# Optimization experiments

Hardware: AMD Instinct MI355X
Metric: run time of the kernel (lower is better)

## Reference

```python
import jax, jax.numpy as jnp
import numpy as np

DIMS = [1024, 2048, 2048, 51]
B, P = 16, 1024


def setup_inputs() -> dict:
    key = jax.random.key(0)
    ks = jax.random.split(key, 1 + 2 * (len(DIMS) - 1))
    inp = {
        "num_pairs": P,
        "classifier_input": jax.random.normal(ks[0], (B, P, DIMS[0]), dtype=jnp.float32),
        "num_batches": B,
    }
    # Linear params, PyTorch-style: W[out, in], b[out]
    for li in range(len(DIMS) - 1):
        fan_in = DIMS[li]
        bound = 1.0 / np.sqrt(fan_in)
        inp[f"W{li}"] = jax.random.uniform(ks[1 + 2 * li], (DIMS[li + 1], fan_in), minval=-bound, maxval=bound, dtype=jnp.float32)
        inp[f"b{li}"] = jax.random.uniform(ks[2 + 2 * li], (DIMS[li + 1],), minval=-bound, maxval=bound, dtype=jnp.float32)
    return inp


def reference(num_pairs, classifier_input, num_batches, W0, b0, W1, b1, W2, b2):
    # Batched MLP over all (num_batches * num_pairs) vectors at once.
    # Original loops per (b, i); math is identical. dropout p=0.0 -> identity.
    x = classifier_input  # [B, P, d_in]
    x = jax.nn.relu(jnp.einsum("bpd,hd->bph", x, W0) + b0)
    x = jax.nn.relu(jnp.einsum("bpd,hd->bph", x, W1) + b1)
    out = jnp.einsum("bpd,od->bpo", x, W2) + b2  # [B, P, n_classes]
    return out
```

## Files before the change

### kernel.cpp

```cpp
#include <hip/hip_runtime.h>
#include <hip/hip_bf16.h>
#include <stdint.h>

typedef __attribute__((ext_vector_type(8))) short short8;
typedef __attribute__((ext_vector_type(8))) uint16_t ushort8;
typedef __attribute__((ext_vector_type(4))) float floatx4;

#define TK 32


__device__ __forceinline__ uint16_t f2bf_bits(float f) {
    uint32_t u = __builtin_bit_cast(uint32_t, f);
    u += 0x7FFFu + ((u >> 16) & 1u);
    return (uint16_t)(u >> 16);
}

__device__ __forceinline__ void async_copy16(const void* g, void* l) {
    auto gp = (const __attribute__((address_space(1))) uint32_t*)(uintptr_t)g;
    auto lp = (__attribute__((address_space(3))) uint32_t*)(uint32_t)(uintptr_t)l;
    __builtin_amdgcn_global_load_lds(gp, lp, 16, 0, 0);
}

__device__ __forceinline__ void cvt8_one(const float* __restrict__ s, uint16_t* __restrict__ d) {
    floatx4 a = *(const floatx4*)(s);
    floatx4 b = *(const floatx4*)(s + 4);
    ushort8 o;
#pragma unroll
    for (int k = 0; k < 4; k++) { o[k] = f2bf_bits(a[k]); o[k + 4] = f2bf_bits(b[k]); }
    *(ushort8*)(d) = o;
}


__global__ void cvt8(const float* __restrict__ src, uint16_t* __restrict__ dst, int n) {
    int i = (blockIdx.x * 256 + threadIdx.x) * 8;
    if (i < n) cvt8_one(src + i, dst + i);
}

__global__ void cvt_weights(const float* __restrict__ W0, const float* __restrict__ W1,
                            const float* __restrict__ W2,
                            uint16_t* __restrict__ o0, uint16_t* __restrict__ o1,
                            uint16_t* __restrict__ o2) {
    int i = (blockIdx.x * 256 + threadIdx.x) * 8;
    if (i < 2097152) {
        cvt8_one(W0 + i, o0 + i);
    } else if (i < 2097152 + 4194304) {
        int j = i - 2097152;
        cvt8_one(W1 + j, o1 + j);
    } else {
        int j = i - 6291456;
        if (j < 131072) {
            int row = j >> 11;
            if (row < 51) cvt8_one(W2 + j, o2 + j);
            else { ushort8 z = {0,0,0,0,0,0,0,0}; *(ushort8*)(o2 + j) = z; }
        }
    }
}

__global__ void init_bias(const float* __restrict__ b2, float* __restrict__ out, int n) {
    int i = blockIdx.x * 256 + threadIdx.x;
    if (i < n) out[i] = b2[i % 51];
}


template <int MI, int NJ, int SPLITK, bool RELU, bool OUTF32, bool ATOMIC>
__global__ __launch_bounds__(256, 2)
void gemm_bt(const uint16_t* __restrict__ A,
             const uint16_t* __restrict__ W,
             const float* __restrict__ bias,
             void* __restrict__ out,
             int M, int N, int lda, int kspan, int ldc, int nstore)
{
    constexpr int TMv = MI * 32;
    constexpr int TNv = NJ * 32;
    constexpr int ACH = TMv / 64;
    constexpr int BCH = TNv / 64;

    __shared__ alignas(16) uint16_t sA[2][TMv * TK];
    __shared__ alignas(16) uint16_t sB[2][TNv * TK];

    const int tid  = threadIdx.x;
    const int wave = tid >> 6;
    const int lane = tid & 63;

    const int f = blockIdx.x;
    int m0, n0, kbeg;
    if constexpr (SPLITK > 1) {
        kbeg = (f % SPLITK) * kspan;
        m0   = (f / SPLITK) * TMv;
        n0   = 0;
    } else {
        kbeg = 0;
        const int xcd = f & 7;
        const int loc = f >> 3;
        const int per = (int)gridDim.x >> 3;
        const int nt  = N / TNv;
        n0 = (loc % nt) * TNv;
        m0 = (xcd * (per / nt) + loc / nt) * TMv;
    }

    floatx4 acc[MI][NJ];
    const floatx4 zero = {0.f, 0.f, 0.f, 0.f};
#pragma unroll
    for (int i = 0; i < MI; i++)
#pragma unroll
        for (int j = 0; j < NJ; j++) acc[i][j] = zero;

    const int wr = (wave >> 1) * MI * 16;
    const int wc = (wave & 1) * NJ * 16;

    const int sr   = lane >> 2;
    const int scol = ((lane & 3) ^ ((lane >> 3) & 3)) * 8;

    const uint16_t* ap[ACH];
    const uint16_t* bp[BCH];
#pragma unroll
    for (int t = 0; t < ACH; t++)
        ap[t] = A + (size_t)(m0 + (wave + 4 * t) * 16 + sr) * lda + kbeg + scol;
#pragma unroll
    for (int t = 0; t < BCH; t++)
        bp[t] = W + (size_t)(n0 + (wave + 4 * t) * 16 + sr) * lda + kbeg + scol;

    auto prefetch = [&](int buf) {
#pragma unroll
        for (int t = 0; t < ACH; t++) {
            async_copy16(ap[t], &sA[buf][(wave + 4 * t) * 512]);
            ap[t] += TK;
        }
#pragma unroll
        for (int t = 0; t < BCH; t++) {
            async_copy16(bp[t], &sB[buf][(wave + 4 * t) * 512]);
            bp[t] += TK;
        }
    };

    const int fm = lane & 15;
    const int slot = ((lane >> 4) ^ ((fm >> 1) & 3)) * 8;

    auto compute = [&](int buf) {
        short8 af[MI], bfr[NJ];
#pragma unroll
        for (int i = 0; i < MI; i++)
            af[i] = *(const short8*)(&sA[buf][(wr + i * 16 + fm) * TK + slot]);
#pragma unroll
        for (int j = 0; j < NJ; j++)
            bfr[j] = *(const short8*)(&sB[buf][(wc + j * 16 + fm) * TK + slot]);
#pragma unroll
        for (int i = 0; i < MI; i++)
#pragma unroll
            for (int j = 0; j < NJ; j++)
                acc[i][j] = __builtin_amdgcn_mfma_f32_16x16x32_bf16(af[i], bfr[j], acc[i][j], 0, 0, 0);
    };

    const int niter = kspan / TK;
    prefetch(0);
    for (int it = 0; it < niter; it += 2) {
        __syncthreads();
        if (it + 1 < niter) prefetch(1);
        compute(0);
        __syncthreads();
        if (it + 2 < niter) prefetch(0);
        compute(1);
    }

    const int cr = (lane >> 4) * 4;
    const int cc = lane & 15;
#pragma unroll
    for (int i = 0; i < MI; i++) {
        const int gmb = m0 + wr + i * 16 + cr;
#pragma unroll
        for (int j = 0; j < NJ; j++) {
            const int gn = n0 + wc + j * 16 + cc;
            if (gn < nstore) {
                float bv = 0.f;
                if constexpr (!ATOMIC) bv = bias[gn];
#pragma unroll
                for (int r = 0; r < 4; r++) {
                    float v = acc[i][j][r] + bv;
                    if (RELU) v = fmaxf(v, 0.f);
                    const size_t idx = (size_t)(gmb + r) * ldc + gn;
                    if constexpr (ATOMIC)      atomicAdd(&((float*)out)[idx], v);
                    else if constexpr (OUTF32) ((float*)out)[idx] = v;
                    else                       ((uint16_t*)out)[idx] = f2bf_bits(v);
                }
            }
        }
    }
}


extern "C" void kernel_launch(void* const* d_in, const int* in_sizes, int n_in,
                              void* d_out, int out_size, void* d_ws, size_t ws_size,
                              hipStream_t stream) {
    (void)in_sizes; (void)n_in; (void)out_size; (void)ws_size;
    const float* X  = (const float*)d_in[1];
    const float* W0 = (const float*)d_in[3];
    const float* b0 = (const float*)d_in[4];
    const float* W1 = (const float*)d_in[5];
    const float* b1 = (const float*)d_in[6];
    const float* W2 = (const float*)d_in[7];
    const float* b2 = (const float*)d_in[8];

    const int M = 16384;

    char* w = (char*)d_ws;
    uint16_t* X0  = (uint16_t*)w; w += (size_t)M * 1024 * 2;
    uint16_t* X1  = (uint16_t*)w; w += (size_t)M * 2048 * 2;
    uint16_t* X2  = (uint16_t*)w; w += (size_t)M * 2048 * 2;
    uint16_t* W0b = (uint16_t*)w; w += (size_t)2048 * 1024 * 2;
    uint16_t* W1b = (uint16_t*)w; w += (size_t)2048 * 2048 * 2;
    uint16_t* W2b = (uint16_t*)w; w += (size_t)64 * 2048 * 2;

    init_bias<<<(M * 51 + 255) / 256, 256, 0, stream>>>(b2, (float*)d_out, M * 51);
    cvt8<<<M * 1024 / 8 / 256, 256, 0, stream>>>(X, X0, M * 1024);
    cvt_weights<<<(2097152 + 4194304 + 131072) / 8 / 256, 256, 0, stream>>>(
        W0, W1, W2, W0b, W1b, W2b);

    gemm_bt<4, 8, 1, true, false, false><<<dim3((M / 128) * (2048 / 256)), 256, 0, stream>>>(
        X0, W0b, b0, X1, M, 2048, 1024, 1024, 2048, 2048);
    gemm_bt<4, 8, 1, true, false, false><<<dim3((M / 128) * (2048 / 256)), 256, 0, stream>>>(
        X1, W1b, b1, X2, M, 2048, 2048, 2048, 2048, 2048);
    gemm_bt<4, 2, 8, false, true, true><<<dim3((M / 128) * 8), 256, 0, stream>>>(
        X2, W2b, nullptr, d_out, M, 64, 2048, 256, 51, 51);
}
```

Before: 401.3 us.

## Use single-buffered TK=64 GEMM loop and replace split-K atomics with partial reduce

The GEMM main loop drops LDS double buffering in favour of a single buffer with a K tile of 64, loading and then computing with two barriers per iteration and a new 8-column XOR swizzle. The final split-K layer now writes per-split partial sums into a workspace buffer that reuses X0, and a separate reduce kernel adds the bias and sums them, replacing the init_bias pass and the fp32 atomics. The aim is fewer barriers per K and no atomic contention. The cost is that global-to-LDS copies no longer overlap MFMA work and an extra kernel launch is added.

```diff
diff --git a/kernel.cpp b/kernel.cpp
--- a/kernel.cpp
+++ b/kernel.cpp
@@ -6,7 +6,7 @@
 typedef __attribute__((ext_vector_type(8))) uint16_t ushort8;
 typedef __attribute__((ext_vector_type(4))) float floatx4;
 
-#define TK 32
+#define TK 64
 
 
 __device__ __forceinline__ uint16_t f2bf_bits(float f) {
@@ -56,13 +56,21 @@
     }
 }
 
-__global__ void init_bias(const float* __restrict__ b2, float* __restrict__ out, int n) {
-    int i = blockIdx.x * 256 + threadIdx.x;
-    if (i < n) out[i] = b2[i % 51];
-}
-
-
-template <int MI, int NJ, int SPLITK, bool RELU, bool OUTF32, bool ATOMIC>
+__global__ void reduce_out(const float* __restrict__ part, const float* __restrict__ b2,
+                           float* __restrict__ out, int M) {
+    int idx = blockIdx.x * 256 + threadIdx.x;
+    int o = idx & 63;
+    if (o < 51) {
+        int m = idx >> 6;
+        float s = b2[o];
+#pragma unroll
+        for (int k = 0; k < 8; k++) s += part[(size_t)k * M * 64 + idx];
+        out[m * 51 + o] = s;
+    }
+}
+
+
+template <int MI, int NJ, int SPLITK, bool RELU, bool PARTIAL>
 __global__ __launch_bounds__(256, 2)
 void gemm_bt(const uint16_t* __restrict__ A,
              const uint16_t* __restrict__ W,
@@ -72,11 +80,11 @@
 {
     constexpr int TMv = MI * 32;
     constexpr int TNv = NJ * 32;
-    constexpr int ACH = TMv / 64;
-    constexpr int BCH = TNv / 64;
-
-    __shared__ alignas(16) uint16_t sA[2][TMv * TK];
-    __shared__ alignas(16) uint16_t sB[2][TNv * TK];
+    constexpr int ACH = TMv / 32;
+    constexpr int BCH = TNv / 32;
+
+    __shared__ alignas(16) uint16_t sA[TMv * TK];
+    __shared__ alignas(16) uint16_t sB[TNv * TK];
 
     const int tid  = threadIdx.x;
     const int wave = tid >> 6;
@@ -84,10 +92,13 @@
 
     const int f = blockIdx.x;
     int m0, n0, kbeg;
+    float* opart = (float*)out;
     if constexpr (SPLITK > 1) {
-        kbeg = (f % SPLITK) * kspan;
-        m0   = (f / SPLITK) * TMv;
+        const int kidx = f & (SPLITK - 1);
+        kbeg = kidx * kspan;
+        m0   = (f >> 3) * TMv;
         n0   = 0;
+        opart += (size_t)kidx * M * ldc;
     } else {
         kbeg = 0;
         const int xcd = f & 7;
@@ -108,58 +119,53 @@
     const int wr = (wave >> 1) * MI * 16;
     const int wc = (wave & 1) * NJ * 16;
 
-    const int sr   = lane >> 2;
-    const int scol = ((lane & 3) ^ ((lane >> 3) & 3)) * 8;
+    const int sr   = lane >> 3;
+    const int scol = ((lane & 7) ^ sr) * 8;
 
     const uint16_t* ap[ACH];
     const uint16_t* bp[BCH];
 #pragma unroll
     for (int t = 0; t < ACH; t++)
-        ap[t] = A + (size_t)(m0 + (wave + 4 * t) * 16 + sr) * lda + kbeg + scol;
+        ap[t] = A + (size_t)(m0 + (wave + 4 * t) * 8 + sr) * lda + kbeg + scol;
 #pragma unroll
     for (int t = 0; t < BCH; t++)
-        bp[t] = W + (size_t)(n0 + (wave + 4 * t) * 16 + sr) * lda + kbeg + scol;
-
-    auto prefetch = [&](int buf) {
+        bp[t] = W + (size_t)(n0 + (wave + 4 * t) * 8 + sr) * lda + kbeg + scol;
+
+    const int fm = lane & 15;
+    const int fr = fm & 7;
+    const int kgb = lane >> 4;
+
+    const int niter = kspan / TK;
+    for (int it = 0; it < niter; it++) {
 #pragma unroll
         for (int t = 0; t < ACH; t++) {
-            async_copy16(ap[t], &sA[buf][(wave + 4 * t) * 512]);
+            async_copy16(ap[t], sA + (wave + 4 * t) * 512);
             ap[t] += TK;
         }
 #pragma unroll
         for (int t = 0; t < BCH; t++) {
-            async_copy16(bp[t], &sB[buf][(wave + 4 * t) * 512]);
+            async_copy16(bp[t], sB + (wave + 4 * t) * 512);
             bp[t] += TK;
         }
-    };
-
-    const int fm = lane & 15;
-    const int slot = ((lane >> 4) ^ ((fm >> 1) & 3)) * 8;
-
-    auto compute = [&](int buf) {
-        short8 af[MI], bfr[NJ];
-#pragma unroll
-        for (int i = 0; i < MI; i++)
-            af[i] = *(const short8*)(&sA[buf][(wr + i * 16 + fm) * TK + slot]);
-#pragma unroll
-        for (int j = 0; j < NJ; j++)
-            bfr[j] = *(const short8*)(&sB[buf][(wc + j * 16 + fm) * TK + slot]);
-#pragma unroll
-        for (int i = 0; i < MI; i++)
+        __syncthreads();
+
+#pragma unroll
+        for (int kk = 0; kk < 2; kk++) {
+            const int slot = ((kgb + 4 * kk) ^ fr) * 8;
+            short8 af[MI], bfr[NJ];
+#pragma unroll
+            for (int i = 0; i < MI; i++)
+                af[i] = *(const short8*)(sA + (wr + i * 16 + fm) * TK + slot);
 #pragma unroll
             for (int j = 0; j < NJ; j++)
-                acc[i][j] = __builtin_amdgcn_mfma_f32_16x16x32_bf16(af[i], bfr[j], acc[i][j], 0, 0, 0);
-    };
-
-    const int niter = kspan / TK;
-    prefetch(0);
-    for (int it = 0; it < niter; it += 2) {
+                bfr[j] = *(const short8*)(sB + (wc + j * 16 + fm) * TK + slot);
+#pragma unroll
+            for (int i = 0; i < MI; i++)
+#pragma unroll
+                for (int j = 0; j < NJ; j++)
+                    acc[i][j] = __builtin_amdgcn_mfma_f32_16x16x32_bf16(af[i], bfr[j], acc[i][j], 0, 0, 0);
+        }
         __syncthreads();
-        if (it + 1 < niter) prefetch(1);
-        compute(0);
-        __syncthreads();
-        if (it + 2 < niter) prefetch(0);
-        compute(1);
     }
 
     const int cr = (lane >> 4) * 4;
@@ -172,15 +178,14 @@
             const int gn = n0 + wc + j * 16 + cc;
             if (gn < nstore) {
                 float bv = 0.f;
-                if constexpr (!ATOMIC) bv = bias[gn];
+                if constexpr (!PARTIAL) bv = bias[gn];
 #pragma unroll
                 for (int r = 0; r < 4; r++) {
                     float v = acc[i][j][r] + bv;
                     if (RELU) v = fmaxf(v, 0.f);
                     const size_t idx = (size_t)(gmb + r) * ldc + gn;
-                    if constexpr (ATOMIC)      atomicAdd(&((float*)out)[idx], v);
-                    else if constexpr (OUTF32) ((float*)out)[idx] = v;
-                    else                       ((uint16_t*)out)[idx] = f2bf_bits(v);
+                    if constexpr (PARTIAL) opart[idx] = v;
+                    else                   ((uint16_t*)out)[idx] = f2bf_bits(v);
                 }
             }
         }
@@ -209,16 +214,17 @@
     uint16_t* W0b = (uint16_t*)w; w += (size_t)2048 * 1024 * 2;
     uint16_t* W1b = (uint16_t*)w; w += (size_t)2048 * 2048 * 2;
     uint16_t* W2b = (uint16_t*)w; w += (size_t)64 * 2048 * 2;
-
-    init_bias<<<(M * 51 + 255) / 256, 256, 0, stream>>>(b2, (float*)d_out, M * 51);
+    float* part = (float*)X0;
+
     cvt8<<<M * 1024 / 8 / 256, 256, 0, stream>>>(X, X0, M * 1024);
     cvt_weights<<<(2097152 + 4194304 + 131072) / 8 / 256, 256, 0, stream>>>(
         W0, W1, W2, W0b, W1b, W2b);
 
-    gemm_bt<4, 8, 1, true, false, false><<<dim3((M / 128) * (2048 / 256)), 256, 0, stream>>>(
+    gemm_bt<4, 8, 1, true, false><<<dim3((M / 128) * (2048 / 256)), 256, 0, stream>>>(
         X0, W0b, b0, X1, M, 2048, 1024, 1024, 2048, 2048);
-    gemm_bt<4, 8, 1, true, false, false><<<dim3((M / 128) * (2048 / 256)), 256, 0, stream>>>(
+    gemm_bt<4, 8, 1, true, false><<<dim3((M / 128) * (2048 / 256)), 256, 0, stream>>>(
         X1, W1b, b1, X2, M, 2048, 2048, 2048, 2048, 2048);
-    gemm_bt<4, 2, 8, false, true, true><<<dim3((M / 128) * 8), 256, 0, stream>>>(
-        X2, W2b, nullptr, d_out, M, 64, 2048, 256, 51, 51);
-}
+    gemm_bt<4, 2, 8, false, true><<<dim3((M / 128) * 8), 256, 0, stream>>>(
+        X2, W2b, nullptr, part, M, 64, 2048, 256, 64, 64);
+    reduce_out<<<M * 64 / 256, 256, 0, stream>>>(part, b2, (float*)d_out, M);
+}
```

Result: faster. 347.8 us (-13.3%).
